# Performance work log

Hardware: AMD Instinct MI355X
Metric: run time of the kernel (lower is better)

## Reference

```python
import jax, jax.numpy as jnp
import numpy as np

T, B = 128, 256      # seq_len, batch
D = 1024             # input_dim (embedding dim)
H = 1024             # hidden_dim
NQ = 8               # n_qubits
V = 32000            # vocab_size
TAGS = 1024          # tagset_size


def setup_inputs() -> dict:
    key = jax.random.key(0)
    ks = jax.random.split(key, 10)
    s = 0.05
    return {
        "sentence": jax.random.randint(ks[0], (T, B), 0, V),
        "emb": jax.random.normal(ks[1], (V, D), jnp.float32) * s,
        # gate order: forget, input, update, output (stacked on leading axis)
        "Wg": jax.random.normal(ks[2], (4, D + H, NQ), jnp.float32) * s,
        "bg": jax.random.normal(ks[3], (4, NQ), jnp.float32) * s,
        "theta": jax.random.normal(ks[4], (4, NQ), jnp.float32) * s,  # trainable RX angles
        "Wp": jax.random.normal(ks[5], (4, NQ, H), jnp.float32) * s,
        "bp": jax.random.normal(ks[6], (4, H), jnp.float32) * s,
        "W_tag": jax.random.normal(ks[7], (H, TAGS), jnp.float32) * s,
        "b_tag": jax.random.normal(ks[8], (TAGS,), jnp.float32) * s,
    }


def reference(sentence, emb, Wg, bg, theta, Wp, bp, W_tag, b_tag):
    embeds = emb[sentence]                      # (T, B, D)
    bsz = embeds.shape[1]
    hidden = Wp.shape[2]

    def step(carry, x):
        hx, cx = carry
        comb = jnp.concatenate([x, hx], axis=1)                       # (B, D+H)
        raw = jnp.einsum('bc,gcq->gbq', comb, Wg) + bg[:, None, :]    # (4, B, NQ)
        # QLayer: RX(x) then trainable RX(theta) per wire on |0>, measure Z
        # -> product state, <Z_i> = cos(raw_i + theta_i)  (exact)
        q = jnp.cos(raw + theta[:, None, :])                          # (4, B, NQ)
        proj = jnp.einsum('gbq,gqh->gbh', q, Wp) + bp[:, None, :]     # (4, B, H)
        f = jax.nn.sigmoid(proj[0])
        i = jax.nn.sigmoid(proj[1])
        g = jnp.tanh(proj[2])
        o = jax.nn.sigmoid(proj[3])
        cx = f * cx + i * g
        hx = o * jnp.tanh(cx)
        return (hx, cx), hx

    hx0 = jnp.zeros((bsz, hidden), embeds.dtype)
    cx0 = jnp.zeros((bsz, hidden), embeds.dtype)
    _, lstm_out = jax.lax.scan(step, (hx0, cx0), embeds)              # (T, B, H)
    tag_logits = lstm_out @ W_tag + b_tag                             # (T, B, TAGS)
    # torch applies log_softmax over dim=1 (the batch axis) -- faithful
    return jax.nn.log_softmax(tag_logits, axis=1)
```

## Files before the change

kernel.cpp:

```cpp
#include <hip/hip_runtime.h>
#include <hip/hip_bf16.h>
#include <stdint.h>

#define T_LEN 128
#define B_SZ  256
#define D_IN  1024
#define H_DIM 1024
#define NQ    8
#define VOCAB 32000
#define TAGS  1024

typedef __attribute__((ext_vector_type(8))) short short8;
typedef __attribute__((ext_vector_type(4))) float f32x4;

__device__ __forceinline__ unsigned short f2bf_bits(float x) {
    __hip_bfloat16 h = __float2bfloat16(x);
    unsigned short u; __builtin_memcpy(&u, &h, 2); return u;
}
__device__ __forceinline__ uint32_t pack_bf2(float a, float b) {
    return (uint32_t)f2bf_bits(a) | ((uint32_t)f2bf_bits(b) << 16);
}
__device__ __forceinline__ float2 unpack_bf2(uint32_t u) {
    float2 r;
    r.x = __uint_as_float(u << 16);
    r.y = __uint_as_float(u & 0xffff0000u);
    return r;
}
__device__ __forceinline__ float sigmoid_f(float x) {
    return 1.f / (1.f + __expf(-x));
}
__device__ __forceinline__ float tanh_f(float x) {
    return 1.f - 2.f / (__expf(2.f * x) + 1.f);
}
__device__ __forceinline__ void gload_lds16(void* lds_base, const void* gptr) {
    __builtin_amdgcn_global_load_lds(
        (__attribute__((address_space(1))) const void*)gptr,
        (__attribute__((address_space(3))) void*)lds_base,
        16, 0, 0);
}

__global__ __launch_bounds__(256) void k_wt_transpose(const float* __restrict__ W,
                                                      __hip_bfloat16* __restrict__ WtT) {
    __shared__ float tile[32][33];
    const int kb = blockIdx.x * 32, nb = blockIdx.y * 32;
    const int r = threadIdx.x >> 5, c = threadIdx.x & 31;
#pragma unroll
    for (int i = 0; i < 4; ++i)
        tile[r + 8 * i][c] = W[(size_t)(kb + r + 8 * i) * TAGS + nb + c];
    __syncthreads();
#pragma unroll
    for (int i = 0; i < 4; ++i)
        WtT[(size_t)(nb + r + 8 * i) * H_DIM + kb + c] = __float2bfloat16(tile[c][r + 8 * i]);
}

__global__ __launch_bounds__(1024) void k_qlstm(
    const int* __restrict__ sent, const float* __restrict__ emb,
    const float* __restrict__ Wg, const float* __restrict__ bg,
    const float* __restrict__ theta, const float* __restrict__ Wp,
    const float* __restrict__ bp, __hip_bfloat16* __restrict__ hb)
{
    __shared__ float comb[2048];
    __shared__ float red[32 * 17];
    __shared__ float qs[32];

    const int tid  = threadIdx.x;
    const int b    = blockIdx.x;
    const int o    = tid & 31;
    const int s    = tid >> 5;
    const int g    = o >> 3, q = o & 7;
    const int lane = tid & 63, wv = tid >> 6;

    uint32_t wg2[32];
#pragma unroll
    for (int j = 0; j < 32; ++j) {
        const int c0 = s * 64 + 2 * j;
        float a = Wg[((size_t)g * 2048 + c0) * 8 + q];
        float bb = Wg[((size_t)g * 2048 + c0 + 1) * 8 + q];
        wg2[j] = pack_bf2(a, bb);
    }
    uint32_t wp2[16];
#pragma unroll
    for (int j = 0; j < 16; ++j) {
        const int gg = j >> 2, jj = j & 3;
        float a = Wp[(size_t)(gg * 8 + 2 * jj) * H_DIM + tid];
        float bb = Wp[(size_t)(gg * 8 + 2 * jj + 1) * H_DIM + tid];
        wp2[j] = pack_bf2(a, bb);
    }
    float bpv[4];
#pragma unroll
    for (int gg = 0; gg < 4; ++gg) bpv[gg] = bp[gg * H_DIM + tid];
    const float bgt = (tid < 32) ? (bg[tid] + theta[tid]) : 0.f;

    float cx = 0.f;
    comb[1024 + tid] = 0.f;
    {
        const int w0 = sent[b];
        comb[tid] = emb[(size_t)w0 * D_IN + tid];
    }
    __syncthreads();

    for (int t = 0; t < T_LEN; ++t) {
        const int tn = (t + 1 < T_LEN) ? (t + 1) : (T_LEN - 1);
        const int wn = sent[tn * B_SZ + b];
        const float xnext = emb[(size_t)wn * D_IN + tid];

        float acc = 0.f;
        const float4* c4 = (const float4*)comb;
#pragma unroll
        for (int i = 0; i < 16; ++i) {
            float4 v = c4[s * 16 + i];
            float2 wa = unpack_bf2(wg2[2 * i]);
            float2 wb = unpack_bf2(wg2[2 * i + 1]);
            acc = fmaf(wa.x, v.x, acc);
            acc = fmaf(wa.y, v.y, acc);
            acc = fmaf(wb.x, v.z, acc);
            acc = fmaf(wb.y, v.w, acc);
        }
        acc += __shfl_xor(acc, 32, 64);
        if (lane < 32) red[lane * 17 + wv] = acc;
        __syncthreads();

        if (tid < 32) {
            float r = bgt;
#pragma unroll
            for (int w = 0; w < 16; ++w) r += red[tid * 17 + w];
            qs[tid] = __cosf(r);
        }
        comb[tid] = xnext;
        __syncthreads();

        const float4* q4 = (const float4*)qs;
        float pj[4];
#pragma unroll
        for (int gg = 0; gg < 4; ++gg) {
            float4 u = q4[2 * gg], v = q4[2 * gg + 1];
            float2 w0 = unpack_bf2(wp2[gg * 4 + 0]);
            float2 w1 = unpack_bf2(wp2[gg * 4 + 1]);
            float2 w2 = unpack_bf2(wp2[gg * 4 + 2]);
            float2 w3 = unpack_bf2(wp2[gg * 4 + 3]);
            pj[gg] = bpv[gg]
                   + u.x * w0.x + u.y * w0.y + u.z * w1.x + u.w * w1.y
                   + v.x * w2.x + v.y * w2.y + v.z * w3.x + v.w * w3.y;
        }
        const float f_ = sigmoid_f(pj[0]);
        const float i_ = sigmoid_f(pj[1]);
        const float g_ = tanh_f(pj[2]);
        const float o_ = sigmoid_f(pj[3]);
        cx = f_ * cx + i_ * g_;
        const float hv = o_ * tanh_f(cx);
        comb[1024 + tid] = hv;
        hb[((size_t)t * B_SZ + b) * H_DIM + tid] = __float2bfloat16(hv);
        __syncthreads();
    }
}

__global__ __launch_bounds__(256) void k_tag_gemm(const __hip_bfloat16* __restrict__ Hb,
                                                  const __hip_bfloat16* __restrict__ WtT,
                                                  float* __restrict__ out)
{
    __shared__ short As[128 * 32];
    __shared__ short Bs[128 * 32];
    const int m0 = blockIdx.x * 128, n0 = blockIdx.y * 128;
    const int tid = threadIdx.x, lane = tid & 63, wid = tid >> 6;
    const int wm = (wid & 1) * 64, wn = (wid >> 1) * 64;
    const int mrow = lane & 15, quad = lane >> 4;

    const short* Hs = (const short*)Hb;
    const short* Ws = (const short*)WtT;

    f32x4 acc[4][4];
#pragma unroll
    for (int mi = 0; mi < 4; ++mi)
#pragma unroll
        for (int ni = 0; ni < 4; ++ni)
            acc[mi][ni] = (f32x4){0.f, 0.f, 0.f, 0.f};

    for (int kt = 0; kt < 32; ++kt) {
        const int k0 = kt * 32;
        __syncthreads();
#pragma unroll
        for (int ch = 0; ch < 2; ++ch) {
            const int chunk = wid + ch * 4;
            const int row = chunk * 16 + (lane >> 2);
            const int kc = (lane & 3) * 8;
            gload_lds16(&As[chunk * 512], &Hs[(size_t)(m0 + row) * H_DIM + k0 + kc]);
            gload_lds16(&Bs[chunk * 512], &Ws[(size_t)(n0 + row) * H_DIM + k0 + kc]);
        }
        __syncthreads();

        short8 afr[4], bfr[4];
#pragma unroll
        for (int mi = 0; mi < 4; ++mi)
            afr[mi] = *(const short8*)&As[(wm + mi * 16 + mrow) * 32 + quad * 8];
#pragma unroll
        for (int ni = 0; ni < 4; ++ni)
            bfr[ni] = *(const short8*)&Bs[(wn + ni * 16 + mrow) * 32 + quad * 8];
#pragma unroll
        for (int mi = 0; mi < 4; ++mi)
#pragma unroll
            for (int ni = 0; ni < 4; ++ni)
                acc[mi][ni] = __builtin_amdgcn_mfma_f32_16x16x32_bf16(
                    afr[mi], bfr[ni], acc[mi][ni], 0, 0, 0);
    }

#pragma unroll
    for (int mi = 0; mi < 4; ++mi)
#pragma unroll
        for (int ni = 0; ni < 4; ++ni)
#pragma unroll
            for (int r = 0; r < 4; ++r) {
                const int grow = m0 + wm + mi * 16 + quad * 4 + r;
                const int gcol = n0 + wn + ni * 16 + mrow;
                out[(size_t)grow * TAGS + gcol] = acc[mi][ni][r];
            }
}

__global__ __launch_bounds__(256) void k_logsoftmax(float* __restrict__ out) {
    const int t = blockIdx.x;
    const int n = blockIdx.y * 256 + threadIdx.x;
    float* base = out + (size_t)t * B_SZ * TAGS + n;
    float m = -1e30f;
    for (int b = 0; b < B_SZ; ++b) m = fmaxf(m, base[(size_t)b * TAGS]);
    float s = 0.f;
    for (int b = 0; b < B_SZ; ++b) s += __expf(base[(size_t)b * TAGS] - m);
    const float lse = m + __logf(s);
    for (int b = 0; b < B_SZ; ++b) base[(size_t)b * TAGS] -= lse;
}

extern "C" void kernel_launch(void* const* d_in, const int* in_sizes, int n_in,
                              void* d_out, int out_size, void* d_ws, size_t ws_size,
                              hipStream_t stream) {
    (void)in_sizes; (void)n_in; (void)out_size; (void)ws_size;
    const int*   sent  = (const int*)d_in[0];
    const float* emb   = (const float*)d_in[1];
    const float* Wg    = (const float*)d_in[2];
    const float* bg    = (const float*)d_in[3];
    const float* theta = (const float*)d_in[4];
    const float* Wp    = (const float*)d_in[5];
    const float* bp    = (const float*)d_in[6];
    const float* Wt    = (const float*)d_in[7];
    float* out = (float*)d_out;

    __hip_bfloat16* hb  = (__hip_bfloat16*)d_ws;
    __hip_bfloat16* WtT = (__hip_bfloat16*)((char*)d_ws + (size_t)64 * 1024 * 1024);

    k_wt_transpose<<<dim3(32, 32), 256, 0, stream>>>(Wt, WtT);
    k_qlstm<<<dim3(B_SZ), 1024, 0, stream>>>(sent, emb, Wg, bg, theta, Wp, bp, hb);
    k_tag_gemm<<<dim3(256, 8), 256, 0, stream>>>(hb, WtT, out);
    k_logsoftmax<<<dim3(T_LEN, 4), 256, 0, stream>>>(out);
}
```

Before: 699.9 us.

## Hoist input-gate projection out of recurrence into separate parallel kernel

Splits the gate pre-activation into an input part (emb·Wg_x + bias + theta), computed for all timesteps up front in a new kernel k_gx, and a recurrent part (h·Wg_h) that stays in the sequential loop. This halves the per-step dot-product work on the critical path, removes the embedding gather from the loop, and replaces the cross-wave LDS reduction plus its extra barrier with full wave shuffle reductions. Weights are now kept in fp32 registers instead of packed bf16, which raises register use. The gx scratch lives in the output buffer before the GEMM overwrites it.

```diff
diff --git a/kernel.cpp b/kernel.cpp
--- a/kernel.cpp
+++ b/kernel.cpp
@@ -13,19 +13,6 @@
 typedef __attribute__((ext_vector_type(8))) short short8;
 typedef __attribute__((ext_vector_type(4))) float f32x4;
 
-__device__ __forceinline__ unsigned short f2bf_bits(float x) {
-    __hip_bfloat16 h = __float2bfloat16(x);
-    unsigned short u; __builtin_memcpy(&u, &h, 2); return u;
-}
-__device__ __forceinline__ uint32_t pack_bf2(float a, float b) {
-    return (uint32_t)f2bf_bits(a) | ((uint32_t)f2bf_bits(b) << 16);
-}
-__device__ __forceinline__ float2 unpack_bf2(uint32_t u) {
-    float2 r;
-    r.x = __uint_as_float(u << 16);
-    r.y = __uint_as_float(u & 0xffff0000u);
-    return r;
-}
 __device__ __forceinline__ float sigmoid_f(float x) {
     return 1.f / (1.f + __expf(-x));
 }
@@ -53,80 +40,123 @@
         WtT[(size_t)(nb + r + 8 * i) * H_DIM + kb + c] = __float2bfloat16(tile[c][r + 8 * i]);
 }
 
-__global__ __launch_bounds__(1024) void k_qlstm(
+#define GX_ROWS 128
+__global__ __launch_bounds__(1024) void k_gx(
     const int* __restrict__ sent, const float* __restrict__ emb,
     const float* __restrict__ Wg, const float* __restrict__ bg,
-    const float* __restrict__ theta, const float* __restrict__ Wp,
-    const float* __restrict__ bp, __hip_bfloat16* __restrict__ hb)
+    const float* __restrict__ theta, float* __restrict__ gx)
 {
-    __shared__ float comb[2048];
-    __shared__ float red[32 * 17];
+    __shared__ float xs[2][1024];
+    const int tid = threadIdx.x, lane = tid & 63, wv = tid >> 6;
+    const int o0 = 2 * wv, o1 = o0 + 1;
+    const int g0 = o0 >> 3, q0 = o0 & 7;
+    const int g1 = o1 >> 3, q1 = o1 & 7;
+
+    float wA[16], wB[16];
+#pragma unroll
+    for (int j = 0; j < 4; ++j)
+#pragma unroll
+        for (int e = 0; e < 4; ++e) {
+            const int c = j * 256 + lane * 4 + e;
+            wA[4 * j + e] = Wg[((size_t)g0 * 2048 + c) * 8 + q0];
+            wB[4 * j + e] = Wg[((size_t)g1 * 2048 + c) * 8 + q1];
+        }
+    const float bt0 = bg[o0] + theta[o0];
+    const float bt1 = bg[o1] + theta[o1];
+
+    const int r0 = blockIdx.x * GX_ROWS;
+    xs[0][tid] = emb[(size_t)sent[r0] * D_IN + tid];
+    __syncthreads();
+
+    int cur = 0;
+    for (int i = 0; i < GX_ROWS; ++i) {
+        const int rn = r0 + ((i + 1 < GX_ROWS) ? (i + 1) : i);
+        const float xnext = emb[(size_t)sent[rn] * D_IN + tid];
+
+        const float4* x4 = (const float4*)xs[cur];
+        float a0 = 0.f, a1 = 0.f;
+#pragma unroll
+        for (int j = 0; j < 4; ++j) {
+            float4 v = x4[j * 64 + lane];
+            a0 = fmaf(wA[4 * j + 0], v.x, a0); a1 = fmaf(wB[4 * j + 0], v.x, a1);
+            a0 = fmaf(wA[4 * j + 1], v.y, a0); a1 = fmaf(wB[4 * j + 1], v.y, a1);
+            a0 = fmaf(wA[4 * j + 2], v.z, a0); a1 = fmaf(wB[4 * j + 2], v.z, a1);
+            a0 = fmaf(wA[4 * j + 3], v.w, a0); a1 = fmaf(wB[4 * j + 3], v.w, a1);
+        }
+#pragma unroll
+        for (int d = 1; d < 64; d <<= 1) {
+            a0 += __shfl_xor(a0, d, 64);
+            a1 += __shfl_xor(a1, d, 64);
+        }
+        xs[cur ^ 1][tid] = xnext;
+        if (lane == 0) {
+            float2 o2; o2.x = a0 + bt0; o2.y = a1 + bt1;
+            *(float2*)&gx[(size_t)(r0 + i) * 32 + o0] = o2;
+        }
+        __syncthreads();
+        cur ^= 1;
+    }
+}
+
+__global__ __launch_bounds__(1024) void k_qlstm(
+    const float* __restrict__ gx, const float* __restrict__ Wg,
+    const float* __restrict__ Wp, const float* __restrict__ bp,
+    __hip_bfloat16* __restrict__ hb)
+{
+    __shared__ float hs[1024];
     __shared__ float qs[32];
-
-    const int tid  = threadIdx.x;
-    const int b    = blockIdx.x;
-    const int o    = tid & 31;
-    const int s    = tid >> 5;
-    const int g    = o >> 3, q = o & 7;
-    const int lane = tid & 63, wv = tid >> 6;
-
-    uint32_t wg2[32];
-#pragma unroll
-    for (int j = 0; j < 32; ++j) {
-        const int c0 = s * 64 + 2 * j;
-        float a = Wg[((size_t)g * 2048 + c0) * 8 + q];
-        float bb = Wg[((size_t)g * 2048 + c0 + 1) * 8 + q];
-        wg2[j] = pack_bf2(a, bb);
-    }
-    uint32_t wp2[16];
-#pragma unroll
-    for (int j = 0; j < 16; ++j) {
-        const int gg = j >> 2, jj = j & 3;
-        float a = Wp[(size_t)(gg * 8 + 2 * jj) * H_DIM + tid];
-        float bb = Wp[(size_t)(gg * 8 + 2 * jj + 1) * H_DIM + tid];
-        wp2[j] = pack_bf2(a, bb);
-    }
+    __shared__ float gxl[T_LEN * 32];
+
+    const int tid = threadIdx.x, lane = tid & 63, wv = tid >> 6;
+    const int b = blockIdx.x;
+    const int o0 = 2 * wv, o1 = o0 + 1;
+    const int g0 = o0 >> 3, q0 = o0 & 7;
+    const int g1 = o1 >> 3, q1 = o1 & 7;
+
+    float wA[16], wB[16];
+#pragma unroll
+    for (int j = 0; j < 4; ++j)
+#pragma unroll
+        for (int e = 0; e < 4; ++e) {
+            const int c = j * 256 + lane * 4 + e;
+            wA[4 * j + e] = Wg[((size_t)g0 * 2048 + 1024 + c) * 8 + q0];
+            wB[4 * j + e] = Wg[((size_t)g1 * 2048 + 1024 + c) * 8 + q1];
+        }
+    float wpv[32];
+#pragma unroll
+    for (int j = 0; j < 32; ++j) wpv[j] = Wp[(size_t)j * H_DIM + tid];
     float bpv[4];
 #pragma unroll
     for (int gg = 0; gg < 4; ++gg) bpv[gg] = bp[gg * H_DIM + tid];
-    const float bgt = (tid < 32) ? (bg[tid] + theta[tid]) : 0.f;
-
+
+#pragma unroll
+    for (int i = tid; i < T_LEN * 32; i += 1024)
+        gxl[i] = gx[((size_t)(i >> 5) * B_SZ + b) * 32 + (i & 31)];
+
+    hs[tid] = 0.f;
     float cx = 0.f;
-    comb[1024 + tid] = 0.f;
-    {
-        const int w0 = sent[b];
-        comb[tid] = emb[(size_t)w0 * D_IN + tid];
-    }
     __syncthreads();
 
     for (int t = 0; t < T_LEN; ++t) {
-        const int tn = (t + 1 < T_LEN) ? (t + 1) : (T_LEN - 1);
-        const int wn = sent[tn * B_SZ + b];
-        const float xnext = emb[(size_t)wn * D_IN + tid];
-
-        float acc = 0.f;
-        const float4* c4 = (const float4*)comb;
-#pragma unroll
-        for (int i = 0; i < 16; ++i) {
-            float4 v = c4[s * 16 + i];
-            float2 wa = unpack_bf2(wg2[2 * i]);
-            float2 wb = unpack_bf2(wg2[2 * i + 1]);
-            acc = fmaf(wa.x, v.x, acc);
-            acc = fmaf(wa.y, v.y, acc);
-            acc = fmaf(wb.x, v.z, acc);
-            acc = fmaf(wb.y, v.w, acc);
-        }
-        acc += __shfl_xor(acc, 32, 64);
-        if (lane < 32) red[lane * 17 + wv] = acc;
-        __syncthreads();
-
-        if (tid < 32) {
-            float r = bgt;
-#pragma unroll
-            for (int w = 0; w < 16; ++w) r += red[tid * 17 + w];
-            qs[tid] = __cosf(r);
-        }
-        comb[tid] = xnext;
+        const float4* h4 = (const float4*)hs;
+        float a0 = 0.f, a1 = 0.f;
+#pragma unroll
+        for (int j = 0; j < 4; ++j) {
+            float4 v = h4[j * 64 + lane];
+            a0 = fmaf(wA[4 * j + 0], v.x, a0); a1 = fmaf(wB[4 * j + 0], v.x, a1);
+            a0 = fmaf(wA[4 * j + 1], v.y, a0); a1 = fmaf(wB[4 * j + 1], v.y, a1);
+            a0 = fmaf(wA[4 * j + 2], v.z, a0); a1 = fmaf(wB[4 * j + 2], v.z, a1);
+            a0 = fmaf(wA[4 * j + 3], v.w, a0); a1 = fmaf(wB[4 * j + 3], v.w, a1);
+        }
+#pragma unroll
+        for (int d = 1; d < 64; d <<= 1) {
+            a0 += __shfl_xor(a0, d, 64);
+            a1 += __shfl_xor(a1, d, 64);
+        }
+        if (lane == 0) {
+            qs[o0] = __cosf(a0 + gxl[t * 32 + o0]);
+            qs[o1] = __cosf(a1 + gxl[t * 32 + o1]);
+        }
         __syncthreads();
 
         const float4* q4 = (const float4*)qs;
@@ -134,13 +164,11 @@
 #pragma unroll
         for (int gg = 0; gg < 4; ++gg) {
             float4 u = q4[2 * gg], v = q4[2 * gg + 1];
-            float2 w0 = unpack_bf2(wp2[gg * 4 + 0]);
-            float2 w1 = unpack_bf2(wp2[gg * 4 + 1]);
-            float2 w2 = unpack_bf2(wp2[gg * 4 + 2]);
-            float2 w3 = unpack_bf2(wp2[gg * 4 + 3]);
             pj[gg] = bpv[gg]
-                   + u.x * w0.x + u.y * w0.y + u.z * w1.x + u.w * w1.y
-                   + v.x * w2.x + v.y * w2.y + v.z * w3.x + v.w * w3.y;
+                   + u.x * wpv[gg * 8 + 0] + u.y * wpv[gg * 8 + 1]
+                   + u.z * wpv[gg * 8 + 2] + u.w * wpv[gg * 8 + 3]
+                   + v.x * wpv[gg * 8 + 4] + v.y * wpv[gg * 8 + 5]
+                   + v.z * wpv[gg * 8 + 6] + v.w * wpv[gg * 8 + 7];
         }
         const float f_ = sigmoid_f(pj[0]);
         const float i_ = sigmoid_f(pj[1]);
@@ -148,7 +176,7 @@
         const float o_ = sigmoid_f(pj[3]);
         cx = f_ * cx + i_ * g_;
         const float hv = o_ * tanh_f(cx);
-        comb[1024 + tid] = hv;
+        hs[tid] = hv;
         hb[((size_t)t * B_SZ + b) * H_DIM + tid] = __float2bfloat16(hv);
         __syncthreads();
     }
@@ -243,9 +271,11 @@
 
     __hip_bfloat16* hb  = (__hip_bfloat16*)d_ws;
     __hip_bfloat16* WtT = (__hip_bfloat16*)((char*)d_ws + (size_t)64 * 1024 * 1024);
+    float* gx = (float*)d_out;
 
     k_wt_transpose<<<dim3(32, 32), 256, 0, stream>>>(Wt, WtT);
-    k_qlstm<<<dim3(B_SZ), 1024, 0, stream>>>(sent, emb, Wg, bg, theta, Wp, bp, hb);
+    k_gx<<<dim3(256), 1024, 0, stream>>>(sent, emb, Wg, bg, theta, gx);
+    k_qlstm<<<dim3(B_SZ), 1024, 0, stream>>>(gx, Wg, Wp, bp, hb);
     k_tag_gemm<<<dim3(256, 8), 256, 0, stream>>>(hb, WtT, out);
     k_logsoftmax<<<dim3(T_LEN, 4), 256, 0, stream>>>(out);
 }
```

Measured after the change: 786.5 us. 12.4% more time.
